# Optimization experiments

Measured on AMD Instinct MI355X. Metric: run time of the kernel, lower is better.

The kernel has to match this reference:

```python
import jax, jax.numpy as jnp
import numpy as np
import math

B = 8192
LAT, COND, OUT = 64, 256, 512
HID, E, NLAYER, GH = 1024, 8, 3, 128
INPUT = LAT + COND          # 320
INTER = LAT + HID           # 1088
EPS = 1e-5


def _ln(x):
    # F.layer_norm(input, input.shape[1:]) -> no affine, eps=1e-5, over last dim
    m = jnp.mean(x, axis=-1, keepdims=True)
    v = jnp.var(x, axis=-1, keepdims=True)
    return (x - m) * jax.lax.rsqrt(v + EPS)


def setup_inputs() -> dict:
    key = jax.random.key(0)
    ks = jax.random.split(key, 24)
    d = {}
    d['z'] = jax.random.normal(ks[0], (B, LAT), jnp.float32)
    d['c'] = jax.random.normal(ks[1], (B, COND), jnp.float32)
    # gate MLP params (PyTorch Linear default init scale ~ 1/sqrt(fan_in))
    gate_dims = [(INPUT, GH), (GH, GH), (GH, E)]
    for i, (fi, fo) in enumerate(gate_dims):
        s = 1.0 / math.sqrt(fi)
        d[f'g{i}_w'] = jax.random.uniform(ks[2 + 2 * i], (fi, fo), jnp.float32, -s, s)
        d[f'g{i}_b'] = jax.random.uniform(ks[3 + 2 * i], (fo,), jnp.float32, -s, s)
    # expert decoder layers: weight [E, in, out], bias [E, out], stdv = 1/sqrt(in)
    for i in range(NLAYER + 1):
        fi = INPUT if i == 0 else INTER
        fo = HID if i != NLAYER else OUT
        s = 1.0 / math.sqrt(fi)
        d[f'w{i}'] = jax.random.uniform(ks[8 + 2 * i], (E, fi, fo), jnp.float32, -s, s)
        d[f'b{i}'] = jax.random.uniform(ks[9 + 2 * i], (E, fo), jnp.float32, -s, s)
    return d


def reference(z, c, g0_w, g0_b, g1_w, g1_b, g2_w, g2_b,
              w0, b0, w1, b1, w2, b2, w3, b3):
    x = jnp.concatenate([z, c], axis=-1)                    # [B, INPUT]
    h = jax.nn.elu(x @ g0_w + g0_b)
    h = jax.nn.elu(h @ g1_w + g1_b)
    coeff = jax.nn.softmax(h @ g2_w + g2_b, axis=-1)        # [B, E]

    layer_out = c
    layers = [(w0, b0, True), (w1, b1, True), (w2, b2, True), (w3, b3, False)]
    for w, b, act in layers:
        inp = _ln(jnp.concatenate([z, layer_out], axis=-1))  # [B, J]
        per = jnp.einsum('bj,ejk->ebk', inp, w)              # per-expert outputs
        out = jnp.einsum('be,ebk->bk', coeff, per) + coeff @ b
        layer_out = jax.nn.elu(out) if act else out
    return layer_out
```

## Files before the change

### kernel.cpp

```cpp
#include <hip/hip_runtime.h>
#include <cstdint>
#include <cstddef>

#define B_ROWS 8192
#define E_EXP  8

typedef unsigned short ushort_t;
typedef short bf16x8 __attribute__((ext_vector_type(8)));
typedef float f32x4  __attribute__((ext_vector_type(4)));

__device__ __forceinline__ ushort_t f2b(float f) {
  union { float f; unsigned int i; } v; v.f = f;
  unsigned int u = v.i;
  unsigned int r = (u + 0x7fffu + ((u >> 16) & 1u)) >> 16;
  return (ushort_t)r;
}
__device__ __forceinline__ float eluf(float x) {
  return x > 0.f ? x : (__expf(x) - 1.f);
}

__global__ void transpose_k(const float* __restrict__ src,
                            ushort_t* __restrict__ dst, int R, int C) {
  __shared__ ushort_t tile[64][65];
  int c0 = blockIdx.x * 64, r0 = blockIdx.y * 64;
  int x = threadIdx.x, y = threadIdx.y;
#pragma unroll
  for (int i = 0; i < 4; ++i)
    tile[y + 16 * i][x] = f2b(src[(size_t)(r0 + y + 16 * i) * C + c0 + x]);
  __syncthreads();
#pragma unroll
  for (int i = 0; i < 4; ++i)
    dst[(size_t)(c0 + y + 16 * i) * R + r0 + x] = tile[x][y + 16 * i];
}

__global__ __launch_bounds__(128) void gate_k(
    const float* __restrict__ z, const float* __restrict__ c,
    const float* __restrict__ g0w, const float* __restrict__ g0b,
    const float* __restrict__ g1w, const float* __restrict__ g1b,
    const float* __restrict__ g2w, const float* __restrict__ g2b,
    float* __restrict__ coeff, float* __restrict__ rat2,
    float* __restrict__ rat4) {
  __shared__ float xs[4][320];
  __shared__ float h1[4][128];
  __shared__ float h2[4][128];
  __shared__ float lg[4][8];
  __shared__ float pr[4][8];
  int t = threadIdx.x;
  int r0 = blockIdx.x * 4;
  for (int idx = t; idx < 4 * 320; idx += 128) {
    int r = idx / 320, j = idx % 320;
    xs[r][j] = (j < 64) ? z[(size_t)(r0 + r) * 64 + j]
                        : c[(size_t)(r0 + r) * 256 + j - 64];
  }
  __syncthreads();
  {
    float bb = g0b[t];
    float a0 = bb, a1 = bb, a2 = bb, a3 = bb;
    for (int j = 0; j < 320; j += 4) {
      float w0 = g0w[j * 128 + t];
      float w1 = g0w[(j + 1) * 128 + t];
      float w2 = g0w[(j + 2) * 128 + t];
      float w3 = g0w[(j + 3) * 128 + t];
      float4 x0 = *(const float4*)&xs[0][j];
      float4 x1 = *(const float4*)&xs[1][j];
      float4 x2 = *(const float4*)&xs[2][j];
      float4 x3 = *(const float4*)&xs[3][j];
      a0 += x0.x * w0 + x0.y * w1 + x0.z * w2 + x0.w * w3;
      a1 += x1.x * w0 + x1.y * w1 + x1.z * w2 + x1.w * w3;
      a2 += x2.x * w0 + x2.y * w1 + x2.z * w2 + x2.w * w3;
      a3 += x3.x * w0 + x3.y * w1 + x3.z * w2 + x3.w * w3;
    }
    h1[0][t] = eluf(a0); h1[1][t] = eluf(a1);
    h1[2][t] = eluf(a2); h1[3][t] = eluf(a3);
  }
  __syncthreads();
  {
    float bb = g1b[t];
    float a0 = bb, a1 = bb, a2 = bb, a3 = bb;
    for (int j = 0; j < 128; j += 4) {
      float w0 = g1w[j * 128 + t];
      float w1 = g1w[(j + 1) * 128 + t];
      float w2 = g1w[(j + 2) * 128 + t];
      float w3 = g1w[(j + 3) * 128 + t];
      float4 x0 = *(const float4*)&h1[0][j];
      float4 x1 = *(const float4*)&h1[1][j];
      float4 x2 = *(const float4*)&h1[2][j];
      float4 x3 = *(const float4*)&h1[3][j];
      a0 += x0.x * w0 + x0.y * w1 + x0.z * w2 + x0.w * w3;
      a1 += x1.x * w0 + x1.y * w1 + x1.z * w2 + x1.w * w3;
      a2 += x2.x * w0 + x2.y * w1 + x2.z * w2 + x2.w * w3;
      a3 += x3.x * w0 + x3.y * w1 + x3.z * w2 + x3.w * w3;
    }
    h2[0][t] = eluf(a0); h2[1][t] = eluf(a1);
    h2[2][t] = eluf(a2); h2[3][t] = eluf(a3);
  }
  __syncthreads();
  if (t < 32) {
    int r = t >> 3, e = t & 7;
    float a = g2b[e];
    for (int j = 0; j < 128; ++j) a += h2[r][j] * g2w[j * 8 + e];
    lg[r][e] = a;
  }
  __syncthreads();
  if (t < 32) {
    int r = t >> 3, e = t & 7;
    float mx = lg[r][0];
#pragma unroll
    for (int i = 1; i < 8; ++i) mx = fmaxf(mx, lg[r][i]);
    float s = 0.f;
#pragma unroll
    for (int i = 0; i < 8; ++i) s += __expf(lg[r][i] - mx);
    float p = __expf(lg[r][e] - mx) / s;
    coeff[(size_t)(r0 + r) * 8 + e] = p;
    pr[r][e] = p;
  }
  __syncthreads();
  if (t < 32) {
    int r = t >> 3, e = t & 7;
    float pe = pr[r][e];
    float ratio = (e < 7) ? pe / fmaxf(pr[r][e + 1], 1e-30f) : pe;
    rat2[(size_t)(r0 + r) * 8 + e] = (e == 3 || e == 7) ? pe : ratio;
    rat4[(size_t)(r0 + r) * 8 + e] = (e & 1) ? pe : ratio;
  }
}

__global__ __launch_bounds__(128) void ln_concat_k(
    const float* __restrict__ z, const float* __restrict__ p0,
    const float* __restrict__ p1, const float* __restrict__ cf,
    const float* __restrict__ bias, ushort_t* __restrict__ out,
    int Pw, int J) {
  int row = blockIdx.x, t = threadIdx.x;
  float vals[9];
  int n = (J + 127) >> 7;
  float cr[8];
  if (p1) {
#pragma unroll
    for (int e = 0; e < 8; ++e) cr[e] = cf[(size_t)row * 8 + e];
  }
  float s = 0.f, s2 = 0.f;
  for (int k = 0; k < n; ++k) {
    int i = t + (k << 7);
    float x = 0.f;
    if (i < J) {
      if (i < 64) {
        x = z[(size_t)row * 64 + i];
      } else if (p1) {
        int j = i - 64;
        float v = p0[(size_t)row * Pw + j] + p1[(size_t)row * Pw + j];
#pragma unroll
        for (int e = 0; e < 8; ++e) v += cr[e] * bias[(size_t)e * Pw + j];
        x = eluf(v);
      } else {
        x = p0[(size_t)row * Pw + i - 64];
      }
    }
    vals[k] = x; s += x; s2 += x * x;
  }
  for (int off = 32; off > 0; off >>= 1) {
    s += __shfl_down(s, off);
    s2 += __shfl_down(s2, off);
  }
  __shared__ float red[4];
  int wid = t >> 6, lane = t & 63;
  if (lane == 0) { red[wid * 2] = s; red[wid * 2 + 1] = s2; }
  __syncthreads();
  float S = red[0] + red[2], S2 = red[1] + red[3];
  float inv = 1.f / (float)J;
  float m = S * inv;
  float var = S2 * inv - m * m;
  float rstd = rsqrtf(var + 1e-5f);
  for (int k = 0; k < n; ++k) {
    int i = t + (k << 7);
    if (i < J) out[(size_t)row * J + i] = f2b((vals[k] - m) * rstd);
  }
}

__device__ __forceinline__ void gload16(const void* g, void* l) {
  __builtin_amdgcn_global_load_lds(
      (const __attribute__((address_space(1))) void*)g,
      (__attribute__((address_space(3))) void*)l, 16, 0, 0);
}

__global__ __launch_bounds__(1024, 1) void moe_gemm_k(
    const ushort_t* __restrict__ inp,
    const ushort_t* __restrict__ wT,
    const float* __restrict__ scales,
    float* __restrict__ outp,
    int J, int K, int ne) {
  const int Kd = E_EXP * J;
  const int nj = J >> 6;
  const int nt = ne * nj;
  __shared__ short As[2][2][16 * 512];
  __shared__ short Wsm[2][2][16 * 512];
  __shared__ float scale_s[256 * 9];

  const int t = threadIdx.x;
  const int w = t >> 6, l = t & 63;
  const int wm = w >> 2, wn = w & 3;
  const int bt = blockIdx.x, ct = blockIdx.y, ez = blockIdx.z;
  const int e0 = ez * ne;
  outp += (size_t)ez * (size_t)B_ROWS * (size_t)K;

#pragma unroll
  for (int i = 0; i < 2; ++i) {
    int idx = t + (i << 10);
    int rw = idx >> 3, e = idx & 7;
    scale_s[rw * 9 + e] = scales[(size_t)(bt * 256 + rw) * 8 + e];
  }

  size_t abase = (size_t)(bt * 256 + w * 16 + (l & 15)) * J + ((l >> 4) * 8);
  size_t wbase = (size_t)(ct * 256 + w * 16 + (l & 15)) * Kd +
                 (size_t)e0 * J + ((l >> 4) * 8);
  int s_acol = 0, s_wcol = 0, sjt = 0;

  auto stageA = [&](int nb, int ks) {
    gload16(inp + abase + s_acol + ks * 32, &As[nb][ks][w * 512]);
  };
  auto stageW = [&](int nb, int ks) {
    gload16(wT + wbase + s_wcol + ks * 32, &Wsm[nb][ks][w * 512]);
  };
  auto advance = [&]() {
    s_wcol += 64;
    if (++sjt == nj) { sjt = 0; s_acol = 0; } else { s_acol += 64; }
  };

  f32x4 acc[4][4];
#pragma unroll
  for (int q = 0; q < 4; ++q)
#pragma unroll
    for (int fn = 0; fn < 4; ++fn) acc[q][fn] = (f32x4){0.f, 0.f, 0.f, 0.f};

#define RDB(ks_)                                                           \
  _Pragma("unroll") for (int fn = 0; fn < 4; ++fn) bf[fn] =                \
      *(const bf16x8*)(&Wsm[b][ks_][(wn * 4 + fn) * 512 + l * 8]);

#define RDA2(d0, d1, ks_, q0)                                              \
  d0 = *(const bf16x8*)(&As[b][ks_][(wm * 4 + (q0)) * 512 + l * 8]);       \
  d1 = *(const bf16x8*)(&As[b][ks_][(wm * 4 + (q0) + 1) * 512 + l * 8]);

#define MM2(q0, a0_, a1_)                                                  \
  __builtin_amdgcn_s_setprio(1);                                           \
  _Pragma("unroll") for (int fn = 0; fn < 4; ++fn) {                       \
    acc[(q0)][fn] = __builtin_amdgcn_mfma_f32_16x16x32_bf16(               \
        a0_, bf[fn], acc[(q0)][fn], 0, 0, 0);                              \
    acc[(q0) + 1][fn] = __builtin_amdgcn_mfma_f32_16x16x32_bf16(           \
        a1_, bf[fn], acc[(q0) + 1][fn], 0, 0, 0);                          \
  }                                                                        \
  __builtin_amdgcn_s_setprio(0);

  stageA(0, 0); stageW(0, 0); stageA(0, 1); stageW(0, 1); advance();
  __syncthreads();

  int cjt = 0, cle = 0;
  for (int tp = 0; tp < nt; ++tp) {
    const int b = tp & 1, nb = b ^ 1;
    const bool more = (tp + 1 < nt);
    bf16x8 bf[4], a0, a1;

    if (more) stageA(nb, 0);
    RDB(0);
    RDA2(a0, a1, 0, 0);
    MM2(0, a0, a1);
    if (more) stageW(nb, 0);
    RDA2(a0, a1, 0, 2);
    MM2(2, a0, a1);
    if (more) asm volatile("s_waitcnt vmcnt(2)" ::: "memory");
    else      asm volatile("s_waitcnt vmcnt(0)" ::: "memory");
    asm volatile("s_barrier" ::: "memory");
    if (more) stageA(nb, 1);
    RDB(1);
    RDA2(a0, a1, 1, 0);
    MM2(0, a0, a1);
    if (more) { stageW(nb, 1); advance(); }
    RDA2(a0, a1, 1, 2);
    MM2(2, a0, a1);
    if (++cjt == nj) {
      cjt = 0;
      int e = e0 + cle;
      ++cle;
#pragma unroll
      for (int q = 0; q < 4; ++q) {
        int rbase = wm * 64 + q * 16 + ((l >> 4) << 2);
#pragma unroll
        for (int rr = 0; rr < 4; ++rr) {
          float rv = scale_s[(rbase + rr) * 9 + e];
#pragma unroll
          for (int fn = 0; fn < 4; ++fn) acc[q][fn][rr] *= rv;
        }
      }
    }
    if (more) asm volatile("s_waitcnt vmcnt(2)" ::: "memory");
    else      asm volatile("s_waitcnt vmcnt(0)" ::: "memory");
    asm volatile("s_barrier" ::: "memory");
  }

#pragma unroll
  for (int q = 0; q < 4; ++q) {
#pragma unroll
    for (int rr = 0; rr < 4; ++rr) {
      int row = wm * 64 + q * 16 + ((l >> 4) << 2) + rr;
      size_t orow = (size_t)(bt * 256 + row) * K + ct * 256;
#pragma unroll
      for (int fn = 0; fn < 4; ++fn) {
        int col = wn * 64 + fn * 16 + (l & 15);
        outp[orow + col] = acc[q][fn][rr];
      }
    }
  }
}

__global__ __launch_bounds__(256) void combine4_k(
    const float* __restrict__ pb, const float* __restrict__ cf,
    const float* __restrict__ bias, float* __restrict__ out, int K) {
  size_t i4 = (size_t)blockIdx.x * 256 + threadIdx.x;
  size_t total = (size_t)B_ROWS * (size_t)K;
  size_t base = i4 * 4;
  if (base >= total) return;
  int row = (int)(base / (size_t)K);
  int col = (int)(base % (size_t)K);
  size_t s4 = total >> 2;
  const f32x4* p4 = (const f32x4*)pb;
  f32x4 v = p4[i4] + p4[i4 + s4] + p4[i4 + 2 * s4] + p4[i4 + 3 * s4];
#pragma unroll
  for (int e = 0; e < 8; ++e) {
    float ce = cf[(size_t)row * 8 + e];
    f32x4 bv = *(const f32x4*)(bias + (size_t)e * K + col);
    v += ce * bv;
  }
  ((f32x4*)out)[i4] = v;
}

extern "C" void kernel_launch(void* const* d_in, const int* in_sizes, int n_in,
                              void* d_out, int out_size, void* d_ws, size_t ws_size,
                              hipStream_t stream) {
  const float* z   = (const float*)d_in[0];
  const float* c   = (const float*)d_in[1];
  const float* g0w = (const float*)d_in[2];
  const float* g0b = (const float*)d_in[3];
  const float* g1w = (const float*)d_in[4];
  const float* g1b = (const float*)d_in[5];
  const float* g2w = (const float*)d_in[6];
  const float* g2b = (const float*)d_in[7];
  const float* w0  = (const float*)d_in[8];
  const float* b0  = (const float*)d_in[9];
  const float* w1  = (const float*)d_in[10];
  const float* b1  = (const float*)d_in[11];
  const float* w2  = (const float*)d_in[12];
  const float* b2  = (const float*)d_in[13];
  const float* w3  = (const float*)d_in[14];
  const float* b3  = (const float*)d_in[15];

  char* ws = (char*)d_ws;
  size_t o = 0;
  auto alloc = [&](size_t bytes) {
    void* p = ws + o;
    o += (bytes + 255) & ~(size_t)255;
    return p;
  };
  ushort_t* wT0 = (ushort_t*)alloc((size_t)2560 * 1024 * 2);
  ushort_t* wT1 = (ushort_t*)alloc((size_t)8704 * 1024 * 2);
  ushort_t* wT2 = (ushort_t*)alloc((size_t)8704 * 1024 * 2);
  ushort_t* wT3 = (ushort_t*)alloc((size_t)8704 * 512 * 2);
  float*    cf   = (float*)alloc((size_t)B_ROWS * 8 * 4);
  float*    rat2 = (float*)alloc((size_t)B_ROWS * 8 * 4);
  float*    rat4 = (float*)alloc((size_t)B_ROWS * 8 * 4);
  ushort_t* inp  = (ushort_t*)alloc((size_t)B_ROWS * 1088 * 2);
  float*    pb   = (float*)alloc((size_t)2 * B_ROWS * 1024 * 4);

  dim3 tb(64, 16);
  transpose_k<<<dim3(1024 / 64, 2560 / 64), tb, 0, stream>>>(w0, wT0, 2560, 1024);
  transpose_k<<<dim3(1024 / 64, 8704 / 64), tb, 0, stream>>>(w1, wT1, 8704, 1024);
  transpose_k<<<dim3(1024 / 64, 8704 / 64), tb, 0, stream>>>(w2, wT2, 8704, 1024);
  transpose_k<<<dim3(512 / 64, 8704 / 64), tb, 0, stream>>>(w3, wT3, 8704, 512);

  gate_k<<<B_ROWS / 4, 128, 0, stream>>>(z, c, g0w, g0b, g1w, g1b, g2w, g2b,
                                         cf, rat2, rat4);

  float* p1v = pb + (size_t)B_ROWS * 1024;

  ln_concat_k<<<B_ROWS, 128, 0, stream>>>(z, c, nullptr, nullptr, nullptr,
                                          inp, 256, 320);
  moe_gemm_k<<<dim3(32, 4, 2), 1024, 0, stream>>>(inp, wT0, rat2, pb, 320, 1024, 4);
  ln_concat_k<<<B_ROWS, 128, 0, stream>>>(z, pb, p1v, cf, b0, inp, 1024, 1088);
  moe_gemm_k<<<dim3(32, 4, 2), 1024, 0, stream>>>(inp, wT1, rat2, pb, 1088, 1024, 4);
  ln_concat_k<<<B_ROWS, 128, 0, stream>>>(z, pb, p1v, cf, b1, inp, 1024, 1088);
  moe_gemm_k<<<dim3(32, 4, 2), 1024, 0, stream>>>(inp, wT2, rat2, pb, 1088, 1024, 4);
  ln_concat_k<<<B_ROWS, 128, 0, stream>>>(z, pb, p1v, cf, b2, inp, 1024, 1088);
  moe_gemm_k<<<dim3(32, 2, 4), 1024, 0, stream>>>(inp, wT3, rat4, pb, 1088, 512, 2);
  combine4_k<<<(B_ROWS * 512) / 1024, 256, 0, stream>>>(pb, cf, b3,
                                                        (float*)d_out, 512);
}
```

Measured before the change: 693.1 us.

## Load MoE GEMM weight fragments directly to registers and halve threads per block

The MoE GEMM kernel now runs 512 threads per block (8 waves, each computing a 128x64 tile) instead of 1024. Weight fragments are read straight from global memory into registers, double-buffered in registers, rather than staged through LDS. Only activations still go through LDS. This removes the weight LDS traffic and half the LDS footprint so two blocks can share a CU, at the cost of many more accumulator registers and uncoalesced 16-byte global weight loads with less reuse per block.

```diff
diff --git a/kernel.cpp b/kernel.cpp
--- a/kernel.cpp
+++ b/kernel.cpp
@@ -181,7 +181,7 @@
       (__attribute__((address_space(3))) void*)l, 16, 0, 0);
 }
 
-__global__ __launch_bounds__(1024, 1) void moe_gemm_k(
+__global__ __launch_bounds__(512, 2) void moe_gemm_k(
     const ushort_t* __restrict__ inp,
     const ushort_t* __restrict__ wT,
     const float* __restrict__ scales,
@@ -191,7 +191,6 @@
   const int nj = J >> 6;
   const int nt = ne * nj;
   __shared__ short As[2][2][16 * 512];
-  __shared__ short Wsm[2][2][16 * 512];
   __shared__ float scale_s[256 * 9];
 
   const int t = threadIdx.x;
@@ -202,108 +201,127 @@
   outp += (size_t)ez * (size_t)B_ROWS * (size_t)K;
 
 #pragma unroll
-  for (int i = 0; i < 2; ++i) {
-    int idx = t + (i << 10);
+  for (int i = 0; i < 4; ++i) {
+    int idx = t + (i << 9);
     int rw = idx >> 3, e = idx & 7;
     scale_s[rw * 9 + e] = scales[(size_t)(bt * 256 + rw) * 8 + e];
   }
 
-  size_t abase = (size_t)(bt * 256 + w * 16 + (l & 15)) * J + ((l >> 4) * 8);
-  size_t wbase = (size_t)(ct * 256 + w * 16 + (l & 15)) * Kd +
-                 (size_t)e0 * J + ((l >> 4) * 8);
+  size_t abase[2];
+#pragma unroll
+  for (int i = 0; i < 2; ++i)
+    abase[i] = (size_t)(bt * 256 + (w * 2 + i) * 16 + (l & 15)) * J +
+               ((l >> 4) * 8);
+  size_t wrow[4];
+#pragma unroll
+  for (int fn = 0; fn < 4; ++fn)
+    wrow[fn] = (size_t)(ct * 256 + wn * 64 + fn * 16 + (l & 15)) * Kd +
+               (size_t)e0 * J + ((l >> 4) * 8);
+
   int s_acol = 0, s_wcol = 0, sjt = 0;
 
-  auto stageA = [&](int nb, int ks) {
-    gload16(inp + abase + s_acol + ks * 32, &As[nb][ks][w * 512]);
-  };
-  auto stageW = [&](int nb, int ks) {
-    gload16(wT + wbase + s_wcol + ks * 32, &Wsm[nb][ks][w * 512]);
+  auto stageA4 = [&](int nb) {
+#pragma unroll
+    for (int ks = 0; ks < 2; ++ks)
+#pragma unroll
+      for (int i = 0; i < 2; ++i)
+        gload16(inp + abase[i] + s_acol + ks * 32,
+                &As[nb][ks][(w * 2 + i) * 512]);
   };
   auto advance = [&]() {
     s_wcol += 64;
     if (++sjt == nj) { sjt = 0; s_acol = 0; } else { s_acol += 64; }
   };
 
-  f32x4 acc[4][4];
-#pragma unroll
-  for (int q = 0; q < 4; ++q)
-#pragma unroll
-    for (int fn = 0; fn < 4; ++fn) acc[q][fn] = (f32x4){0.f, 0.f, 0.f, 0.f};
-
-#define RDB(ks_)                                                           \
-  _Pragma("unroll") for (int fn = 0; fn < 4; ++fn) bf[fn] =                \
-      *(const bf16x8*)(&Wsm[b][ks_][(wn * 4 + fn) * 512 + l * 8]);
-
-#define RDA2(d0, d1, ks_, q0)                                              \
-  d0 = *(const bf16x8*)(&As[b][ks_][(wm * 4 + (q0)) * 512 + l * 8]);       \
-  d1 = *(const bf16x8*)(&As[b][ks_][(wm * 4 + (q0) + 1) * 512 + l * 8]);
-
-#define MM2(q0, a0_, a1_)                                                  \
+#define LOADW(dst)                                                         \
+  _Pragma("unroll") for (int ks = 0; ks < 2; ++ks)                         \
+      _Pragma("unroll") for (int fn = 0; fn < 4; ++fn) dst[ks][fn] =       \
+          *(const bf16x8*)(wT + wrow[fn] + s_wcol + ks * 32);
+
+#define RD_A(dst, b_, ks_, MB)                                             \
+  _Pragma("unroll") for (int q = 0; q < 4; ++q) dst[q] =                   \
+      *(const bf16x8*)(&As[b_][ks_][(wm * 8 + (MB) + q) * 512 + l * 8]);
+
+#define MM16(MB, AF, BF)                                                   \
   __builtin_amdgcn_s_setprio(1);                                           \
-  _Pragma("unroll") for (int fn = 0; fn < 4; ++fn) {                       \
-    acc[(q0)][fn] = __builtin_amdgcn_mfma_f32_16x16x32_bf16(               \
-        a0_, bf[fn], acc[(q0)][fn], 0, 0, 0);                              \
-    acc[(q0) + 1][fn] = __builtin_amdgcn_mfma_f32_16x16x32_bf16(           \
-        a1_, bf[fn], acc[(q0) + 1][fn], 0, 0, 0);                          \
-  }                                                                        \
+  _Pragma("unroll") for (int q = 0; q < 4; ++q)                            \
+      _Pragma("unroll") for (int fn = 0; fn < 4; ++fn) acc[(MB) + q][fn] = \
+          __builtin_amdgcn_mfma_f32_16x16x32_bf16(AF[q], BF[fn],           \
+                                                  acc[(MB) + q][fn], 0, 0, 0); \
   __builtin_amdgcn_s_setprio(0);
 
-  stageA(0, 0); stageW(0, 0); stageA(0, 1); stageW(0, 1); advance();
-  __syncthreads();
+#define COMPUTE(b_, WF)                                                    \
+  {                                                                        \
+    bf16x8 af[4];                                                          \
+    RD_A(af, b_, 0, 0); MM16(0, af, WF[0]);                                \
+    RD_A(af, b_, 0, 4); MM16(4, af, WF[0]);                                \
+    RD_A(af, b_, 1, 0); MM16(0, af, WF[1]);                                \
+    RD_A(af, b_, 1, 4); MM16(4, af, WF[1]);                                \
+  }
+
+  f32x4 acc[8][4];
+#pragma unroll
+  for (int fm = 0; fm < 8; ++fm)
+#pragma unroll
+    for (int fn = 0; fn < 4; ++fn) acc[fm][fn] = (f32x4){0.f, 0.f, 0.f, 0.f};
+
+  bf16x8 wfA[2][4], wfB[2][4];
 
   int cjt = 0, cle = 0;
-  for (int tp = 0; tp < nt; ++tp) {
-    const int b = tp & 1, nb = b ^ 1;
-    const bool more = (tp + 1 < nt);
-    bf16x8 bf[4], a0, a1;
-
-    if (more) stageA(nb, 0);
-    RDB(0);
-    RDA2(a0, a1, 0, 0);
-    MM2(0, a0, a1);
-    if (more) stageW(nb, 0);
-    RDA2(a0, a1, 0, 2);
-    MM2(2, a0, a1);
-    if (more) asm volatile("s_waitcnt vmcnt(2)" ::: "memory");
-    else      asm volatile("s_waitcnt vmcnt(0)" ::: "memory");
-    asm volatile("s_barrier" ::: "memory");
-    if (more) stageA(nb, 1);
-    RDB(1);
-    RDA2(a0, a1, 1, 0);
-    MM2(0, a0, a1);
-    if (more) { stageW(nb, 1); advance(); }
-    RDA2(a0, a1, 1, 2);
-    MM2(2, a0, a1);
+  auto boundary = [&]() {
     if (++cjt == nj) {
       cjt = 0;
       int e = e0 + cle;
       ++cle;
 #pragma unroll
-      for (int q = 0; q < 4; ++q) {
-        int rbase = wm * 64 + q * 16 + ((l >> 4) << 2);
+      for (int fi = 0; fi < 8; ++fi) {
+        int rbase = wm * 128 + fi * 16 + ((l >> 4) << 2);
 #pragma unroll
         for (int rr = 0; rr < 4; ++rr) {
           float rv = scale_s[(rbase + rr) * 9 + e];
 #pragma unroll
-          for (int fn = 0; fn < 4; ++fn) acc[q][fn][rr] *= rv;
+          for (int fn = 0; fn < 4; ++fn) acc[fi][fn][rr] *= rv;
         }
       }
     }
-    if (more) asm volatile("s_waitcnt vmcnt(2)" ::: "memory");
-    else      asm volatile("s_waitcnt vmcnt(0)" ::: "memory");
+  };
+
+  stageA4(0);
+  LOADW(wfA);
+  advance();
+  __syncthreads();
+
+  for (int tp = 0; tp < nt; tp += 2) {
+    const bool m2 = (tp + 2 < nt);
+    stageA4(1);
+    LOADW(wfB);
+    advance();
+    COMPUTE(0, wfA);
+    boundary();
+    asm volatile("s_waitcnt vmcnt(8)" ::: "memory");
     asm volatile("s_barrier" ::: "memory");
-  }
-
-#pragma unroll
-  for (int q = 0; q < 4; ++q) {
+    if (m2) {
+      stageA4(0);
+      LOADW(wfA);
+      advance();
+    }
+    COMPUTE(1, wfB);
+    boundary();
+    if (m2) asm volatile("s_waitcnt vmcnt(8)" ::: "memory");
+    else    asm volatile("s_waitcnt vmcnt(0)" ::: "memory");
+    asm volatile("s_barrier" ::: "memory");
+  }
+
+#pragma unroll
+  for (int fi = 0; fi < 8; ++fi) {
 #pragma unroll
     for (int rr = 0; rr < 4; ++rr) {
-      int row = wm * 64 + q * 16 + ((l >> 4) << 2) + rr;
+      int row = wm * 128 + fi * 16 + ((l >> 4) << 2) + rr;
       size_t orow = (size_t)(bt * 256 + row) * K + ct * 256;
 #pragma unroll
       for (int fn = 0; fn < 4; ++fn) {
         int col = wn * 64 + fn * 16 + (l & 15);
-        outp[orow + col] = acc[q][fn][rr];
+        outp[orow + col] = acc[fi][fn][rr];
       }
     }
   }
@@ -380,13 +398,13 @@
 
   ln_concat_k<<<B_ROWS, 128, 0, stream>>>(z, c, nullptr, nullptr, nullptr,
                                           inp, 256, 320);
-  moe_gemm_k<<<dim3(32, 4, 2), 1024, 0, stream>>>(inp, wT0, rat2, pb, 320, 1024, 4);
+  moe_gemm_k<<<dim3(32, 4, 2), 512, 0, stream>>>(inp, wT0, rat2, pb, 320, 1024, 4);
   ln_concat_k<<<B_ROWS, 128, 0, stream>>>(z, pb, p1v, cf, b0, inp, 1024, 1088);
-  moe_gemm_k<<<dim3(32, 4, 2), 1024, 0, stream>>>(inp, wT1, rat2, pb, 1088, 1024, 4);
+  moe_gemm_k<<<dim3(32, 4, 2), 512, 0, stream>>>(inp, wT1, rat2, pb, 1088, 1024, 4);
   ln_concat_k<<<B_ROWS, 128, 0, stream>>>(z, pb, p1v, cf, b1, inp, 1024, 1088);
-  moe_gemm_k<<<dim3(32, 4, 2), 1024, 0, stream>>>(inp, wT2, rat2, pb, 1088, 1024, 4);
+  moe_gemm_k<<<dim3(32, 4, 2), 512, 0, stream>>>(inp, wT2, rat2, pb, 1088, 1024, 4);
   ln_concat_k<<<B_ROWS, 128, 0, stream>>>(z, pb, p1v, cf, b2, inp, 1024, 1088);
-  moe_gemm_k<<<dim3(32, 2, 4), 1024, 0, stream>>>(inp, wT3, rat4, pb, 1088, 512, 2);
+  moe_gemm_k<<<dim3(32, 2, 4), 512, 0, stream>>>(inp, wT3, rat4, pb, 1088, 512, 2);
   combine4_k<<<(B_ROWS * 512) / 1024, 256, 0, stream>>>(pb, cf, b3,
                                                         (float*)d_out, 512);
 }
```

Result: slower. 1.146 ms (+65.3%).
